# Optimization experiments

Measured on AMD Instinct MI355X. Metric: run time of the kernel, lower is better.

## Reference

```python
import jax, jax.numpy as jnp
import numpy as np

B, H, W, C = 16, 64, 64, 512
HEADS, WS, SHIFT = 16, 8, 4
N = WS * WS            # tokens per window
HID = 4 * C            # mlp hidden


def _buffers():
    # Swin-V2 log-spaced continuous relative coords table [1, 2ws-1, 2ws-1, 2]
    rc = np.arange(-(WS - 1), WS, dtype=np.float32)
    table = np.stack(np.meshgrid(rc, rc, indexing='ij'), axis=-1)[None]
    table = table / (WS - 1) * 8.0
    table = np.sign(table) * np.log2(np.abs(table) + 1.0) / np.log2(8.0)
    # relative position index [N, N]
    coords = np.stack(np.meshgrid(np.arange(WS), np.arange(WS), indexing='ij')).reshape(2, -1)
    rel = (coords[:, :, None] - coords[:, None, :]).transpose(1, 2, 0)
    rel[..., 0] += WS - 1
    rel[..., 1] += WS - 1
    rel[..., 0] *= 2 * WS - 1
    idx = rel.sum(-1).astype(np.int32)
    # shifted-window attention mask [nW, N, N]
    img = np.zeros((H, W), dtype=np.float32)
    sl = (slice(0, -WS), slice(-WS, -SHIFT), slice(-SHIFT, None))
    cnt = 0
    for hs in sl:
        for ws_ in sl:
            img[hs, ws_] = cnt
            cnt += 1
    mw = img.reshape(H // WS, WS, W // WS, WS).transpose(0, 2, 1, 3).reshape(-1, N)
    am = mw[:, None, :] - mw[:, :, None]
    am = np.where(am != 0, np.float32(-100.0), np.float32(0.0)).astype(np.float32)
    return table.astype(np.float32), idx, am


def setup_inputs() -> dict:
    key = jax.random.key(0)
    ks = jax.random.split(key, 8)
    table, idx, am = _buffers()
    p = lambda k, s: jax.random.normal(k, s, jnp.float32) * 0.02
    return {
        'x': jax.random.normal(ks[0], (B, H * W, C), jnp.float32),
        'qkv_w': p(ks[1], (3 * C, C)),
        'q_bias': jnp.zeros((C,), jnp.float32),
        'v_bias': jnp.zeros((C,), jnp.float32),
        'logit_scale': jnp.full((HEADS, 1, 1), np.log(10.0), jnp.float32),
        'cpb_w1': p(ks[2], (512, 2)),
        'cpb_b1': jnp.zeros((512,), jnp.float32),
        'cpb_w2': p(ks[3], (HEADS, 512)),
        'proj_w': p(ks[4], (C, C)),
        'proj_b': jnp.zeros((C,), jnp.float32),
        'norm1_g': jnp.ones((C,), jnp.float32),
        'norm1_b': jnp.zeros((C,), jnp.float32),
        'norm2_g': jnp.ones((C,), jnp.float32),
        'norm2_b': jnp.zeros((C,), jnp.float32),
        'fc1_w': p(ks[5], (HID, C)),
        'fc1_b': jnp.zeros((HID,), jnp.float32),
        'fc2_w': p(ks[6], (C, HID)),
        'fc2_b': jnp.zeros((C,), jnp.float32),
        'coords_table': jnp.asarray(table),
        'attn_mask': jnp.asarray(am),
        'rel_pos_index': jnp.asarray(idx),
    }


def _layernorm(x, g, b):
    m = x.mean(-1, keepdims=True)
    v = ((x - m) ** 2).mean(-1, keepdims=True)
    return (x - m) / jnp.sqrt(v + 1e-5) * g + b


def reference(x, qkv_w, q_bias, v_bias, logit_scale, cpb_w1, cpb_b1, cpb_w2,
              proj_w, proj_b, norm1_g, norm1_b, norm2_g, norm2_b,
              fc1_w, fc1_b, fc2_w, fc2_b, coords_table, attn_mask, rel_pos_index):
    Bsz, L, Cd = x.shape
    d = Cd // HEADS
    shortcut = x
    # cyclic shift + window partition: [B*nW, N, C]
    xr = jnp.roll(x.reshape(Bsz, H, W, Cd), (-SHIFT, -SHIFT), axis=(1, 2))
    xw = xr.reshape(Bsz, H // WS, WS, W // WS, WS, Cd).transpose(0, 1, 3, 2, 4, 5).reshape(-1, N, Cd)
    B_ = xw.shape[0]
    nW = B_ // Bsz
    # qkv with q/v-only bias
    qkv_bias = jnp.concatenate([q_bias, jnp.zeros_like(v_bias), v_bias])
    qkv = (xw @ qkv_w.T + qkv_bias).reshape(B_, N, 3, HEADS, d).transpose(2, 0, 3, 1, 4)
    q, k, v = qkv[0], qkv[1], qkv[2]  # [B_, h, N, d]
    # cosine attention with learned clamped logit scale
    qn = q / jnp.maximum(jnp.linalg.norm(q, axis=-1, keepdims=True), 1e-12)
    kn = k / jnp.maximum(jnp.linalg.norm(k, axis=-1, keepdims=True), 1e-12)
    scale = jnp.exp(jnp.minimum(logit_scale, jnp.log(jnp.float32(100.0))))
    attn = jnp.einsum('bhnd,bhmd->bhnm', qn, kn) * scale
    # CPB MLP relative position bias
    tbl = jax.nn.relu(coords_table @ cpb_w1.T + cpb_b1) @ cpb_w2.T  # [1,2ws-1,2ws-1,h]
    rpb = tbl.reshape(-1, HEADS)[rel_pos_index.reshape(-1)].reshape(N, N, HEADS).transpose(2, 0, 1)
    attn = attn + 16.0 * jax.nn.sigmoid(rpb)[None]
    # shift mask
    attn = (attn.reshape(Bsz, nW, HEADS, N, N) + attn_mask[None, :, None]).reshape(B_, HEADS, N, N)
    attn = jax.nn.softmax(attn, axis=-1)
    out = jnp.einsum('bhnm,bhmd->bhnd', attn, v).transpose(0, 2, 1, 3).reshape(B_, N, Cd)
    out = out @ proj_w.T + proj_b
    # window reverse + reverse shift
    out = out.reshape(Bsz, H // WS, W // WS, WS, WS, Cd).transpose(0, 1, 3, 2, 4, 5).reshape(Bsz, H, W, Cd)
    out = jnp.roll(out, (SHIFT, SHIFT), axis=(1, 2)).reshape(Bsz, L, Cd)
    # Swin-V2 post-norm residuals
    x1 = shortcut + _layernorm(out, norm1_g, norm1_b)
    mlp = jax.nn.gelu(x1 @ fc1_w.T + fc1_b, approximate=False) @ fc2_w.T + fc2_b
    return x1 + _layernorm(mlp, norm2_g, norm2_b)
```

## Files before the change

kernel.cpp:

```cpp
#include <hip/hip_runtime.h>
#include <hip/hip_bf16.h>
#include <math.h>

#define BB     16
#define HH     64
#define WWID   64
#define CCH    512
#define HEADS  16
#define NTOK   64
#define DDIM   32
#define NWIN   64
#define LL     (HH*WWID)
#define MTOT   (BB*LL)
#define BWIN   (BB*NWIN)
#define HIDN   2048
#define SHIFT_ 4

typedef unsigned short u16;
using bf16x8 = __attribute__((ext_vector_type(8))) short;
using f32x4  = __attribute__((ext_vector_type(4))) float;
using f32x16 = __attribute__((ext_vector_type(16))) float;

__device__ __forceinline__ u16 f2bf(float f) {
  union { float f; unsigned u; } v; v.f = f;
  unsigned r = v.u + 0x7fffu + ((v.u >> 16) & 1u);
  return (u16)(r >> 16);
}
__device__ __forceinline__ float bf2f(unsigned h) {
  union { unsigned u; float f; } v; v.u = h << 16;
  return v.f;
}

__device__ __forceinline__ void gload16(const void* g, void* l) {
  __builtin_amdgcn_global_load_lds((const __attribute__((address_space(1))) void*)g,
                                   (__attribute__((address_space(3))) void*)l, 16, 0, 0);
}

__device__ __forceinline__ int win2orig(int b_, int n) {
  int b = b_ >> 6, wi = b_ & 63;
  int hs = (wi >> 3) * 8 + (n >> 3);
  int ws = (wi & 7) * 8 + (n & 7);
  int hq = (hs + SHIFT_) & 63;
  int wq = (ws + SHIFT_) & 63;
  return b * LL + hq * WWID + wq;
}

__global__ void cvt_k(const float* __restrict__ s, u16* __restrict__ d, int n) {
  int i = blockIdx.x * 256 + threadIdx.x;
  if (i < n) d[i] = f2bf(s[i]);
}

__global__ void cpb_k(const float* __restrict__ ct, const float* __restrict__ w1,
                      const float* __restrict__ b1, const float* __restrict__ w2,
                      float* __restrict__ t2) {
  int t = blockIdx.x * 256 + threadIdx.x;
  if (t >= 225 * 16) return;
  int rr = t >> 4, h = t & 15;
  float c0 = ct[rr * 2], c1 = ct[rr * 2 + 1];
  float acc = 0.f;
  for (int j = 0; j < 512; j++) {
    float hv = fmaxf(w1[j * 2] * c0 + w1[j * 2 + 1] * c1 + b1[j], 0.f);
    acc += hv * w2[h * 512 + j];
  }
  t2[t] = acc;
}

__global__ void bias_k(const float* __restrict__ t2, const int* __restrict__ rpi,
                       float* __restrict__ b16) {
  int t = blockIdx.x * 256 + threadIdx.x;
  int nm = t & 4095;
  int h = t >> 12;
  float v = t2[rpi[nm] * 16 + h];
  b16[t] = 16.0f / (1.0f + __expf(-v));
}

__global__ void scale_k(const float* __restrict__ ls, float* __restrict__ sc) {
  int t = threadIdx.x;
  if (t < HEADS) sc[t] = __expf(fminf(ls[t], 4.6051701859880914f));
}

__global__ __launch_bounds__(256) void xw_k(const float* __restrict__ x, u16* __restrict__ xw) {
  int t = blockIdx.x * 256 + threadIdx.x;
  int row = t >> 6;
  int col = (t & 63) * 8;
  const float* src = x + (size_t)win2orig(row >> 6, row & 63) * CCH + col;
  float4 a = *(const float4*)src;
  float4 b = *(const float4*)(src + 4);
  u16 o[8] = {f2bf(a.x), f2bf(a.y), f2bf(a.z), f2bf(a.w),
              f2bf(b.x), f2bf(b.y), f2bf(b.z), f2bf(b.w)};
  *(uint4*)(xw + (size_t)row * CCH + col) = *(const uint4*)o;
}

template<int MODE, int NBN>
__global__ __launch_bounds__(256, 2) void gemm256_k(
    const u16* __restrict__ A, const u16* __restrict__ Bw,
    const float* __restrict__ bias,
    const float* __restrict__ qbias, const float* __restrict__ vbias,
    u16* __restrict__ o0, u16* __restrict__ o1, u16* __restrict__ o2,
    int K, int mchunk)
{
  __shared__ __align__(16) u16 smem[2 * 12288];
  const int t = threadIdx.x;
  const int lin = blockIdx.x;
  const int xcd = lin & 7;
  const int j = lin >> 3;
  const int m0 = (xcd * mchunk + j / NBN) * 256;
  const int n0 = (j % NBN) * 128;
  const int lane = t & 63;
  const int wv = t >> 6;
  const int wm = (wv & 1) * 128;
  const int wn = (wv >> 1) * 64;
  const int l31 = lane & 31;
  const int khalf = lane >> 5;
  const int sw = lane & 3;

  const int swcol = (((t & 3) ^ ((t >> 2) & 3)) * 8);
  const u16* aP[4]; int aL[4];
  #pragma unroll
  for (int i = 0; i < 4; i++) {
    aP[i] = A + (size_t)(m0 + i * 64 + (t >> 2)) * K + swcol;
    aL[i] = i * 4096 + wv * 1024;
  }
  const u16* bP[2]; int bL[2];
  #pragma unroll
  for (int i = 0; i < 2; i++) {
    bP[i] = Bw + (size_t)(n0 + i * 64 + (t >> 2)) * K + swcol;
    bL[i] = 16384 + i * 4096 + wv * 1024;
  }

  f32x16 acc[4][2] = {};

  {
    char* base = (char*)smem;
    #pragma unroll
    for (int i = 0; i < 4; i++) gload16(aP[i], base + aL[i]);
    #pragma unroll
    for (int i = 0; i < 2; i++) gload16(bP[i], base + bL[i]);
  }
  __syncthreads();

  int cur = 0;
  for (int k0 = 0; k0 < K; k0 += 32) {
    if (k0 + 32 < K) {
      char* base = (char*)smem + (cur ^ 1) * 24576;
      #pragma unroll
      for (int i = 0; i < 4; i++) gload16(aP[i] + k0 + 32, base + aL[i]);
      #pragma unroll
      for (int i = 0; i < 2; i++) gload16(bP[i] + k0 + 32, base + bL[i]);
    }
    const u16* Ab = (const u16*)((const char*)smem + cur * 24576);
    const u16* Bb = Ab + 8192;
    #pragma unroll
    for (int ks = 0; ks < 2; ks++) {
      const int kc = (ks * 2 + khalf) ^ sw;
      bf16x8 af[4], bf[2];
      #pragma unroll
      for (int mt = 0; mt < 4; mt++)
        af[mt] = *(const bf16x8*)&Ab[(wm + mt * 32 + l31) * 32 + kc * 8];
      #pragma unroll
      for (int nt = 0; nt < 2; nt++)
        bf[nt] = *(const bf16x8*)&Bb[(wn + nt * 32 + l31) * 32 + kc * 8];
      #pragma unroll
      for (int mt = 0; mt < 4; mt++)
        #pragma unroll
        for (int nt = 0; nt < 2; nt++)
          acc[mt][nt] = __builtin_amdgcn_mfma_f32_32x32x16_bf16(bf[nt], af[mt], acc[mt][nt], 0, 0, 0);
    }
    __syncthreads();
    cur ^= 1;
  }

  const int part = n0 >> 9;
  u16* qkvdst = (MODE == 0) ? (part == 0 ? o0 : (part == 1 ? o1 : o2)) : o0;
  #pragma unroll
  for (int mt = 0; mt < 4; mt++) {
    const int grow = m0 + wm + mt * 32 + l31;
    size_t rowbase;
    if (MODE == 0) {
      int b_ = grow >> 6, n = grow & 63;
      rowbase = ((size_t)b_ * HEADS) * (NTOK * DDIM) + (size_t)n * DDIM;
    } else if (MODE == 1) {
      rowbase = (size_t)win2orig(grow >> 6, grow & 63) * CCH;
    } else if (MODE == 2) {
      rowbase = (size_t)grow * HIDN;
    } else {
      rowbase = (size_t)grow * CCH;
    }
    #pragma unroll
    for (int nt = 0; nt < 2; nt++)
      #pragma unroll
      for (int g = 0; g < 4; g++) {
        const int nb = n0 + wn + nt * 32 + 8 * g + 4 * khalf;
        float v0 = acc[mt][nt][g * 4 + 0];
        float v1 = acc[mt][nt][g * 4 + 1];
        float v2 = acc[mt][nt][g * 4 + 2];
        float v3 = acc[mt][nt][g * 4 + 3];
        union { u16 o[4]; uint2 u; } pk;
        if (MODE == 0) {
          const int cc = nb & 511;
          if (part == 0) {
            float4 b4 = *(const float4*)(qbias + cc);
            v0 += b4.x; v1 += b4.y; v2 += b4.z; v3 += b4.w;
          } else if (part == 2) {
            float4 b4 = *(const float4*)(vbias + cc);
            v0 += b4.x; v1 += b4.y; v2 += b4.z; v3 += b4.w;
          }
          const int hh = cc >> 5, dd = cc & 31;
          pk.o[0] = f2bf(v0); pk.o[1] = f2bf(v1); pk.o[2] = f2bf(v2); pk.o[3] = f2bf(v3);
          *(uint2*)(qkvdst + rowbase + (size_t)hh * (NTOK * DDIM) + dd) = pk.u;
        } else {
          float4 b4 = *(const float4*)(bias + nb);
          v0 += b4.x; v1 += b4.y; v2 += b4.z; v3 += b4.w;
          if (MODE == 2) {
            v0 = 0.5f * v0 * (1.0f + erff(v0 * 0.70710678118654752f));
            v1 = 0.5f * v1 * (1.0f + erff(v1 * 0.70710678118654752f));
            v2 = 0.5f * v2 * (1.0f + erff(v2 * 0.70710678118654752f));
            v3 = 0.5f * v3 * (1.0f + erff(v3 * 0.70710678118654752f));
          }
          pk.o[0] = f2bf(v0); pk.o[1] = f2bf(v1); pk.o[2] = f2bf(v2); pk.o[3] = f2bf(v3);
          *(uint2*)(o0 + rowbase + nb) = pk.u;
        }
      }
  }
}

__global__ __launch_bounds__(64) void attn_k(
    const u16* __restrict__ qb, const u16* __restrict__ kb, const u16* __restrict__ vb,
    const float* __restrict__ bias16, const float* __restrict__ scale,
    const float* __restrict__ amask, u16* __restrict__ attn_out)
{
  __shared__ u16 Pmat[64][72];
  __shared__ u16 vT[32][72];

  int bh = blockIdx.x;
  int b_ = bh >> 4, h = bh & 15;
  int wi = b_ & 63;
  int lane = threadIdx.x;
  int l15 = lane & 15, quad = lane >> 4;
  const u16* qs = qb + (size_t)bh * (NTOK * DDIM);
  const u16* ks = kb + (size_t)bh * (NTOK * DDIM);
  const u16* vs = vb + (size_t)bh * (NTOK * DDIM);

  bf16x8 qf[4], kf[4];
  #pragma unroll
  for (int mt = 0; mt < 4; mt++) {
    qf[mt] = *(const bf16x8*)(qs + (mt * 16 + l15) * DDIM + quad * 8);
    kf[mt] = *(const bf16x8*)(ks + (mt * 16 + l15) * DDIM + quad * 8);
  }
  #pragma unroll
  for (int mt = 0; mt < 4; mt++) {
    float sq = 0.f, sk = 0.f;
    #pragma unroll
    for (int jj = 0; jj < 8; jj++) {
      float a = bf2f((u16)qf[mt][jj]); sq += a * a;
      float b = bf2f((u16)kf[mt][jj]); sk += b * b;
    }
    sq += __shfl_xor(sq, 16); sq += __shfl_xor(sq, 32);
    sk += __shfl_xor(sk, 16); sk += __shfl_xor(sk, 32);
    float iq = 1.f / fmaxf(sqrtf(sq), 1e-12f);
    float ik = 1.f / fmaxf(sqrtf(sk), 1e-12f);
    #pragma unroll
    for (int jj = 0; jj < 8; jj++) {
      qf[mt][jj] = (short)f2bf(bf2f((u16)qf[mt][jj]) * iq);
      kf[mt][jj] = (short)f2bf(bf2f((u16)kf[mt][jj]) * ik);
    }
  }
  f32x4 s[4][4];
  #pragma unroll
  for (int mt = 0; mt < 4; mt++)
    #pragma unroll
    for (int nt = 0; nt < 4; nt++) {
      f32x4 c = {0.f, 0.f, 0.f, 0.f};
      s[mt][nt] = __builtin_amdgcn_mfma_f32_16x16x32_bf16(qf[mt], kf[nt], c, 0, 0, 0);
    }
  #pragma unroll
  for (int d8 = 0; d8 < 4; d8++) {
    bf16x8 vv = *(const bf16x8*)(vs + lane * DDIM + d8 * 8);
    #pragma unroll
    for (int jj = 0; jj < 8; jj++) vT[d8 * 8 + jj][lane] = (u16)vv[jj];
  }

  float sc = scale[h];
  float rinv[4][4];
  const float* bbase = bias16 + (size_t)h * 4096;
  const float* mbase = amask + (size_t)wi * 4096;
  #pragma unroll
  for (int mt = 0; mt < 4; mt++) {
    #pragma unroll
    for (int i = 0; i < 4; i++) {
      int row = mt * 16 + quad * 4 + i;
      const float* bro = bbase + row * 64;
      const float* mro = mbase + row * 64;
      float p[4];
      float mx = -1e30f;
      #pragma unroll
      for (int nt = 0; nt < 4; nt++) {
        int col = nt * 16 + l15;
        float vv = s[mt][nt][i] * sc + bro[col] + mro[col];
        p[nt] = vv;
        mx = fmaxf(mx, vv);
      }
      mx = fmaxf(mx, __shfl_xor(mx, 1));
      mx = fmaxf(mx, __shfl_xor(mx, 2));
      mx = fmaxf(mx, __shfl_xor(mx, 4));
      mx = fmaxf(mx, __shfl_xor(mx, 8));
      float sum = 0.f;
      #pragma unroll
      for (int nt = 0; nt < 4; nt++) {
        float e = __expf(p[nt] - mx);
        p[nt] = e;
        sum += e;
      }
      sum += __shfl_xor(sum, 1);
      sum += __shfl_xor(sum, 2);
      sum += __shfl_xor(sum, 4);
      sum += __shfl_xor(sum, 8);
      rinv[mt][i] = 1.f / sum;
      #pragma unroll
      for (int nt = 0; nt < 4; nt++)
        Pmat[row][nt * 16 + l15] = f2bf(p[nt]);
    }
  }
  __syncthreads();

  f32x4 oacc[4][2] = {};
  #pragma unroll
  for (int ks2 = 0; ks2 < 2; ks2++) {
    bf16x8 pf[4], vf[2];
    #pragma unroll
    for (int mt = 0; mt < 4; mt++)
      pf[mt] = *(const bf16x8*)&Pmat[mt * 16 + l15][ks2 * 32 + quad * 8];
    #pragma unroll
    for (int nt = 0; nt < 2; nt++)
      vf[nt] = *(const bf16x8*)&vT[nt * 16 + l15][ks2 * 32 + quad * 8];
    #pragma unroll
    for (int mt = 0; mt < 4; mt++)
      #pragma unroll
      for (int nt = 0; nt < 2; nt++)
        oacc[mt][nt] = __builtin_amdgcn_mfma_f32_16x16x32_bf16(pf[mt], vf[nt], oacc[mt][nt], 0, 0, 0);
  }
  #pragma unroll
  for (int mt = 0; mt < 4; mt++)
    #pragma unroll
    for (int nt = 0; nt < 2; nt++)
      #pragma unroll
      for (int i = 0; i < 4; i++) {
        int n = mt * 16 + quad * 4 + i;
        int d = nt * 16 + l15;
        float val = oacc[mt][nt][i] * rinv[mt][i];
        attn_out[(size_t)(b_ * 64 + n) * CCH + h * DDIM + d] = f2bf(val);
      }
}

__global__ __launch_bounds__(256) void ln_res_k(
    const float* __restrict__ xin, const u16* __restrict__ pin,
    const float* __restrict__ gam, const float* __restrict__ bet,
    float* __restrict__ x1f, u16* __restrict__ x1b)
{
  int row = blockIdx.x * 4 + (threadIdx.x >> 6);
  int lane = threadIdx.x & 63;
  size_t base = (size_t)row * CCH + lane * 8;
  uint4 u = *(const uint4*)(pin + base);
  unsigned w[4] = {u.x, u.y, u.z, u.w};
  float pv[8];
  #pragma unroll
  for (int j = 0; j < 4; j++) {
    pv[j * 2] = bf2f(w[j] & 0xffffu);
    pv[j * 2 + 1] = bf2f(w[j] >> 16);
  }
  const float* xr = xin + base;
  float s = 0.f, sq = 0.f;
  #pragma unroll
  for (int j = 0; j < 8; j++) { s += pv[j]; sq += pv[j] * pv[j]; }
  #pragma unroll
  for (int o = 32; o > 0; o >>= 1) { s += __shfl_xor(s, o, 64); sq += __shfl_xor(sq, o, 64); }
  float mean = s * (1.0f / 512.0f);
  float var = sq * (1.0f / 512.0f) - mean * mean;
  float rstd = rsqrtf(var + 1e-5f);
  #pragma unroll
  for (int j = 0; j < 8; j++) {
    int c = lane * 8 + j;
    float val = xr[j] + (pv[j] - mean) * rstd * gam[c] + bet[c];
    x1f[base + j] = val;
    x1b[base + j] = f2bf(val);
  }
}

__global__ __launch_bounds__(256) void ln_fin_k(
    const u16* __restrict__ mlp, const float* __restrict__ gam,
    const float* __restrict__ bet, float* __restrict__ io)
{
  int row = blockIdx.x * 4 + (threadIdx.x >> 6);
  int lane = threadIdx.x & 63;
  size_t base = (size_t)row * CCH + lane * 8;
  uint4 u = *(const uint4*)(mlp + base);
  unsigned w[4] = {u.x, u.y, u.z, u.w};
  float pv[8];
  #pragma unroll
  for (int j = 0; j < 4; j++) {
    pv[j * 2] = bf2f(w[j] & 0xffffu);
    pv[j * 2 + 1] = bf2f(w[j] >> 16);
  }
  float s = 0.f, sq = 0.f;
  #pragma unroll
  for (int j = 0; j < 8; j++) { s += pv[j]; sq += pv[j] * pv[j]; }
  #pragma unroll
  for (int o = 32; o > 0; o >>= 1) { s += __shfl_xor(s, o, 64); sq += __shfl_xor(sq, o, 64); }
  float mean = s * (1.0f / 512.0f);
  float var = sq * (1.0f / 512.0f) - mean * mean;
  float rstd = rsqrtf(var + 1e-5f);
  #pragma unroll
  for (int j = 0; j < 8; j++) {
    int c = lane * 8 + j;
    io[base + j] = io[base + j] + (pv[j] - mean) * rstd * gam[c] + bet[c];
  }
}

#define OFF_Q     ((size_t)0)
#define OFF_K     ((size_t)67108864)
#define OFF_V     ((size_t)134217728)
#define OFF_ATTN  ((size_t)201326592)
#define OFF_X1B   ((size_t)268435456)
#define OFF_WQKV  ((size_t)335544320)
#define OFF_WPROJ ((size_t)337117184)
#define OFF_WFC1  ((size_t)337641472)
#define OFF_WFC2  ((size_t)339738624)
#define OFF_T2    ((size_t)341835776)
#define OFF_B16   ((size_t)341852160)
#define OFF_SC    ((size_t)342114304)

extern "C" void kernel_launch(void* const* d_in, const int* in_sizes, int n_in,
                              void* d_out, int out_size, void* d_ws, size_t ws_size,
                              hipStream_t stream) {
  const float* x        = (const float*)d_in[0];
  const float* qkv_w    = (const float*)d_in[1];
  const float* q_bias   = (const float*)d_in[2];
  const float* v_bias   = (const float*)d_in[3];
  const float* lscale   = (const float*)d_in[4];
  const float* cpb_w1   = (const float*)d_in[5];
  const float* cpb_b1   = (const float*)d_in[6];
  const float* cpb_w2   = (const float*)d_in[7];
  const float* proj_w   = (const float*)d_in[8];
  const float* proj_b   = (const float*)d_in[9];
  const float* n1g      = (const float*)d_in[10];
  const float* n1b      = (const float*)d_in[11];
  const float* n2g      = (const float*)d_in[12];
  const float* n2b      = (const float*)d_in[13];
  const float* fc1_w    = (const float*)d_in[14];
  const float* fc1_b    = (const float*)d_in[15];
  const float* fc2_w    = (const float*)d_in[16];
  const float* fc2_b    = (const float*)d_in[17];
  const float* ctab     = (const float*)d_in[18];
  const float* amask    = (const float*)d_in[19];
  const int*   rpi      = (const int*)d_in[20];

  char* ws = (char*)d_ws;
  float* outp = (float*)d_out;

  u16*   q_buf    = (u16*)(ws + OFF_Q);
  u16*   k_buf    = (u16*)(ws + OFF_K);
  u16*   v_buf    = (u16*)(ws + OFF_V);
  u16*   proj_out = (u16*)(ws + OFF_Q);
  u16*   hid      = (u16*)(ws + OFF_Q);
  u16*   xw       = (u16*)(ws + OFF_ATTN);
  u16*   attn_out = (u16*)(ws + OFF_ATTN);
  u16*   mlp_out  = (u16*)(ws + OFF_ATTN);
  u16*   x1b      = (u16*)(ws + OFF_X1B);
  u16*   wqkv     = (u16*)(ws + OFF_WQKV);
  u16*   wproj    = (u16*)(ws + OFF_WPROJ);
  u16*   wfc1     = (u16*)(ws + OFF_WFC1);
  u16*   wfc2     = (u16*)(ws + OFF_WFC2);
  float* t2       = (float*)(ws + OFF_T2);
  float* b16      = (float*)(ws + OFF_B16);
  float* scbuf    = (float*)(ws + OFF_SC);

  cvt_k<<<(1536 * 512 + 255) / 256, 256, 0, stream>>>(qkv_w, wqkv, 1536 * 512);
  cvt_k<<<(512 * 512 + 255) / 256, 256, 0, stream>>>(proj_w, wproj, 512 * 512);
  cvt_k<<<(2048 * 512 + 255) / 256, 256, 0, stream>>>(fc1_w, wfc1, 2048 * 512);
  cvt_k<<<(512 * 2048 + 255) / 256, 256, 0, stream>>>(fc2_w, wfc2, 512 * 2048);
  cpb_k<<<15, 256, 0, stream>>>(ctab, cpb_w1, cpb_b1, cpb_w2, t2);
  bias_k<<<256, 256, 0, stream>>>(t2, rpi, b16);
  scale_k<<<1, 64, 0, stream>>>(lscale, scbuf);

  xw_k<<<MTOT * 64 / 256, 256, 0, stream>>>(x, xw);
  gemm256_k<0, 12><<<256 * 12, 256, 0, stream>>>(
      xw, wqkv, nullptr, q_bias, v_bias, q_buf, k_buf, v_buf, 512, 32);
  attn_k<<<BWIN * HEADS, 64, 0, stream>>>(q_buf, k_buf, v_buf, b16, scbuf, amask, attn_out);
  gemm256_k<1, 4><<<256 * 4, 256, 0, stream>>>(
      attn_out, wproj, proj_b, nullptr, nullptr, proj_out, nullptr, nullptr, 512, 32);
  ln_res_k<<<MTOT / 4, 256, 0, stream>>>(x, proj_out, n1g, n1b, outp, x1b);
  for (int half = 0; half < 2; half++) {
    const u16* a1 = x1b + (size_t)half * (MTOT / 2) * CCH;
    u16* m1 = mlp_out + (size_t)half * (MTOT / 2) * CCH;
    gemm256_k<2, 16><<<128 * 16, 256, 0, stream>>>(
        a1, wfc1, fc1_b, nullptr, nullptr, hid, nullptr, nullptr, 512, 16);
    gemm256_k<3, 4><<<128 * 4, 256, 0, stream>>>(
        hid, wfc2, fc2_b, nullptr, nullptr, m1, nullptr, nullptr, 2048, 16);
  }
  ln_fin_k<<<MTOT / 4, 256, 0, stream>>>(mlp_out, n2g, n2b, outp);
}
```

Baseline: 1.268 ms.

## Triple-buffer GEMM K-loop with single barrier and widen epilogue stores via permlane swap

The shared GEMM kernel moves from a double-buffered K loop with two barriers per step to a three-stage LDS ring. Loads run two tiles ahead, with an explicit vmcnt wait and one barrier per iteration. The epilogue packs bf16 pairs and uses v_permlane32_swap to gather contiguous 8-element segments, so each lane issues 16-byte stores instead of 8-byte ones. LDS use per block grows by half (to 72KB), which may limit the two-blocks-per-CU target, and the hand-written waitcnt relies on the compiler's load ordering.

```diff
diff --git a/kernel.cpp b/kernel.cpp
--- a/kernel.cpp
+++ b/kernel.cpp
@@ -99,7 +99,7 @@
     u16* __restrict__ o0, u16* __restrict__ o1, u16* __restrict__ o2,
     int K, int mchunk)
 {
-  __shared__ __align__(16) u16 smem[2 * 12288];
+  __shared__ __align__(16) u16 smem[3 * 12288];
   const int t = threadIdx.x;
   const int lin = blockIdx.x;
   const int xcd = lin & 7;
@@ -130,25 +130,26 @@
 
   f32x16 acc[4][2] = {};
 
-  {
-    char* base = (char*)smem;
-    #pragma unroll
-    for (int i = 0; i < 4; i++) gload16(aP[i], base + aL[i]);
-    #pragma unroll
-    for (int i = 0; i < 2; i++) gload16(bP[i], base + bL[i]);
-  }
-  __syncthreads();
-
-  int cur = 0;
-  for (int k0 = 0; k0 < K; k0 += 32) {
-    if (k0 + 32 < K) {
-      char* base = (char*)smem + (cur ^ 1) * 24576;
-      #pragma unroll
-      for (int i = 0; i < 4; i++) gload16(aP[i] + k0 + 32, base + aL[i]);
-      #pragma unroll
-      for (int i = 0; i < 2; i++) gload16(bP[i] + k0 + 32, base + bL[i]);
-    }
-    const u16* Ab = (const u16*)((const char*)smem + cur * 24576);
+  auto stage = [&](int k0, int bi) {
+    char* base = (char*)smem + bi * 24576;
+    #pragma unroll
+    for (int i = 0; i < 4; i++) gload16(aP[i] + k0, base + aL[i]);
+    #pragma unroll
+    for (int i = 0; i < 2; i++) gload16(bP[i] + k0, base + bL[i]);
+  };
+
+  const int NT = K >> 5;
+  stage(0, 0);
+  stage(32, 1);
+
+  for (int it = 0; it < NT; ++it) {
+    if (it + 1 < NT) asm volatile("s_waitcnt vmcnt(6)" ::: "memory");
+    else             asm volatile("s_waitcnt vmcnt(0)" ::: "memory");
+    __builtin_amdgcn_s_barrier();
+    asm volatile("" ::: "memory");
+    if (it + 2 < NT) stage((it + 2) << 5, (it + 2) % 3);
+
+    const u16* Ab = (const u16*)((const char*)smem + (it % 3) * 24576);
     const u16* Bb = Ab + 8192;
     #pragma unroll
     for (int ks = 0; ks < 2; ks++) {
@@ -166,8 +167,6 @@
         for (int nt = 0; nt < 2; nt++)
           acc[mt][nt] = __builtin_amdgcn_mfma_f32_32x32x16_bf16(bf[nt], af[mt], acc[mt][nt], 0, 0, 0);
     }
-    __syncthreads();
-    cur ^= 1;
   }
 
   const int part = n0 >> 9;
@@ -187,15 +186,16 @@
       rowbase = (size_t)grow * CCH;
     }
     #pragma unroll
-    for (int nt = 0; nt < 2; nt++)
+    for (int nt = 0; nt < 2; nt++) {
+      const int cb = n0 + wn + nt * 32;
+      unsigned U[4], W[4];
       #pragma unroll
       for (int g = 0; g < 4; g++) {
-        const int nb = n0 + wn + nt * 32 + 8 * g + 4 * khalf;
+        const int nb = cb + 8 * g + 4 * khalf;
         float v0 = acc[mt][nt][g * 4 + 0];
         float v1 = acc[mt][nt][g * 4 + 1];
         float v2 = acc[mt][nt][g * 4 + 2];
         float v3 = acc[mt][nt][g * 4 + 3];
-        union { u16 o[4]; uint2 u; } pk;
         if (MODE == 0) {
           const int cc = nb & 511;
           if (part == 0) {
@@ -205,9 +205,6 @@
             float4 b4 = *(const float4*)(vbias + cc);
             v0 += b4.x; v1 += b4.y; v2 += b4.z; v3 += b4.w;
           }
-          const int hh = cc >> 5, dd = cc & 31;
-          pk.o[0] = f2bf(v0); pk.o[1] = f2bf(v1); pk.o[2] = f2bf(v2); pk.o[3] = f2bf(v3);
-          *(uint2*)(qkvdst + rowbase + (size_t)hh * (NTOK * DDIM) + dd) = pk.u;
         } else {
           float4 b4 = *(const float4*)(bias + nb);
           v0 += b4.x; v1 += b4.y; v2 += b4.z; v3 += b4.w;
@@ -217,10 +214,26 @@
             v2 = 0.5f * v2 * (1.0f + erff(v2 * 0.70710678118654752f));
             v3 = 0.5f * v3 * (1.0f + erff(v3 * 0.70710678118654752f));
           }
-          pk.o[0] = f2bf(v0); pk.o[1] = f2bf(v1); pk.o[2] = f2bf(v2); pk.o[3] = f2bf(v3);
-          *(uint2*)(o0 + rowbase + nb) = pk.u;
         }
+        U[g] = (unsigned)f2bf(v0) | ((unsigned)f2bf(v1) << 16);
+        W[g] = (unsigned)f2bf(v2) | ((unsigned)f2bf(v3) << 16);
       }
+      asm volatile("v_permlane32_swap_b32 %0, %1" : "+v"(U[0]), "+v"(U[1]));
+      asm volatile("v_permlane32_swap_b32 %0, %1" : "+v"(W[0]), "+v"(W[1]));
+      asm volatile("v_permlane32_swap_b32 %0, %1" : "+v"(U[2]), "+v"(U[3]));
+      asm volatile("v_permlane32_swap_b32 %0, %1" : "+v"(W[2]), "+v"(W[3]));
+      uint4 s1 = make_uint4(U[0], W[0], U[1], W[1]);
+      uint4 s2 = make_uint4(U[2], W[2], U[3], W[3]);
+      if (MODE == 0) {
+        const int cc1 = (cb & 511) + 8 * khalf;
+        const int cc2 = cc1 + 16;
+        *(uint4*)(qkvdst + rowbase + (size_t)(cc1 >> 5) * (NTOK * DDIM) + (cc1 & 31)) = s1;
+        *(uint4*)(qkvdst + rowbase + (size_t)(cc2 >> 5) * (NTOK * DDIM) + (cc2 & 31)) = s2;
+      } else {
+        *(uint4*)(o0 + rowbase + cb + 8 * khalf) = s1;
+        *(uint4*)(o0 + rowbase + cb + 16 + 8 * khalf) = s2;
+      }
+    }
   }
 }
 
```

After: 1.150 ms. -9.3%, faster.
